# Kernel tuning notes

Measured on AMD Instinct MI355X. Metric: run time of the kernel, lower is better.

## Reference

```python
import jax, jax.numpy as jnp
import numpy as np

EPS = 1e-5  # torch LayerNorm default


def _ln(x, g, b):
    m = jnp.mean(x, axis=-1, keepdims=True)
    v = jnp.var(x, axis=-1, keepdims=True)
    return (x - m) * jax.lax.rsqrt(v + EPS) * g + b


def _attn(x, ctx, wq, wk, wv, wo, bo, num_heads):
    # weights stored [in, out]; equivalent to torch Linear (y = x @ W^T + b)
    B, T, _ = x.shape
    S = ctx.shape[1]
    E = wq.shape[1]
    hd = E // num_heads
    q = (x @ wq).reshape(B, T, num_heads, hd)
    k = (ctx @ wk).reshape(B, S, num_heads, hd)
    v = (ctx @ wv).reshape(B, S, num_heads, hd)
    scores = jnp.einsum('bthd,bshd->bhts', q, k) / np.sqrt(hd).astype(x.dtype)
    p = jax.nn.softmax(scores, axis=-1)
    o = jnp.einsum('bhts,bshd->bthd', p, v).reshape(B, T, E)
    return o @ wo + bo


def _ffn(x, w1, b1, w2, b2):
    h = jax.nn.gelu(x @ w1 + b1, approximate=False)  # torch nn.GELU default is exact
    return h @ w2 + b2  # Dropout(0.1) is identity in eval mode


def setup_inputs() -> dict:
    key = jax.random.key(0)
    H, CD, FF = 1024, 768, 4096
    ks = jax.random.split(key, 20)
    s = 0.02
    inp = {
        'x': jax.random.normal(ks[0], (4, 1024, H), jnp.float32),
        'context': jax.random.normal(ks[1], (4, 77, CD), jnp.float32),
        # self-attention params
        'sq_w': jax.random.normal(ks[2], (H, H), jnp.float32) * s,
        'sk_w': jax.random.normal(ks[3], (H, H), jnp.float32) * s,
        'sv_w': jax.random.normal(ks[4], (H, H), jnp.float32) * s,
        'so_w': jax.random.normal(ks[5], (H, H), jnp.float32) * s,
        'so_b': jnp.zeros((H,), jnp.float32),
        # cross-attention params
        'cq_w': jax.random.normal(ks[6], (H, H), jnp.float32) * s,
        'ck_w': jax.random.normal(ks[7], (CD, H), jnp.float32) * s,
        'cv_w': jax.random.normal(ks[8], (CD, H), jnp.float32) * s,
        'co_w': jax.random.normal(ks[9], (H, H), jnp.float32) * s,
        'co_b': jnp.zeros((H,), jnp.float32),
        # layer norms 1-4
        'n1_g': jnp.ones((H,), jnp.float32), 'n1_b': jnp.zeros((H,), jnp.float32),
        'n2_g': jnp.ones((H,), jnp.float32), 'n2_b': jnp.zeros((H,), jnp.float32),
        'n3_g': jnp.ones((H,), jnp.float32), 'n3_b': jnp.zeros((H,), jnp.float32),
        'n4_g': jnp.ones((H,), jnp.float32), 'n4_b': jnp.zeros((H,), jnp.float32),
        # FFNs
        'f1_w1': jax.random.normal(ks[10], (H, FF), jnp.float32) * s,
        'f1_b1': jnp.zeros((FF,), jnp.float32),
        'f1_w2': jax.random.normal(ks[11], (FF, H), jnp.float32) * s,
        'f1_b2': jnp.zeros((H,), jnp.float32),
        'f2_w1': jax.random.normal(ks[12], (H, FF), jnp.float32) * s,
        'f2_b1': jnp.zeros((FF,), jnp.float32),
        'f2_w2': jax.random.normal(ks[13], (FF, H), jnp.float32) * s,
        'f2_b2': jnp.zeros((H,), jnp.float32),
    }
    return inp


def reference(x, context,
              sq_w, sk_w, sv_w, so_w, so_b,
              cq_w, ck_w, cv_w, co_w, co_b,
              n1_g, n1_b, n2_g, n2_b, n3_g, n3_b, n4_g, n4_b,
              f1_w1, f1_b1, f1_w2, f1_b2,
              f2_w1, f2_b1, f2_w2, f2_b2):
    NUM_HEADS = 16
    # self-attention branch
    x = _attn(_ln(x, n1_g, n1_b), _ln(x, n1_g, n1_b), sq_w, sk_w, sv_w, so_w, so_b, NUM_HEADS) + x
    x = _ffn(_ln(x, n2_g, n2_b), f1_w1, f1_b1, f1_w2, f1_b2) + x
    # cross-attention branch
    x = _attn(_ln(x, n3_g, n3_b), context, cq_w, ck_w, cv_w, co_w, co_b, NUM_HEADS) + x
    x = _ffn(_ln(x, n4_g, n4_b), f2_w1, f2_b1, f2_w2, f2_b2) + x
    return x
```

## Files before the change

kernel.cpp:

```cpp
#include <hip/hip_runtime.h>
#include <cstdint>
#include <cstddef>

typedef unsigned short u16;
typedef __attribute__((ext_vector_type(8))) short short8;
typedef __attribute__((ext_vector_type(4))) float floatx4;

typedef const __attribute__((address_space(1))) void g_void;
typedef __attribute__((address_space(3))) void l_void;

__device__ __forceinline__ float b2f(u16 u) {
    union { unsigned int i; float f; } v; v.i = ((unsigned int)u) << 16; return v.f;
}
__device__ __forceinline__ u16 f2b(float f) {
    union { float f; unsigned int i; } v; v.f = f;
    unsigned int x = v.i;
    return (u16)((x + 0x7fffu + ((x >> 16) & 1u)) >> 16);
}
__device__ __forceinline__ float gelu_exact(float x) {
    return 0.5f * x * (1.0f + erff(x * 0.70710678118654752440f));
}

__global__ void sniff_kernel(const u16* __restrict__ x, int* __restrict__ flag) {
    int lane = threadIdx.x;
    int sane = 0;
    for (int i = lane * 2; i < 4096; i += 128) {
        int e = (x[i] >> 7) & 0xff;
        if (e >= 100 && e <= 140) sane++;
    }
#pragma unroll
    for (int off = 32; off; off >>= 1) sane += __shfl_xor(sane, off, 64);
    if (lane == 0) *flag = (sane * 2 >= 2048) ? 0 : 1;
}

__global__ __launch_bounds__(256) void cvt_bf_kernel(const void* __restrict__ in,
                                                     u16* __restrict__ out, int n4,
                                                     const int* __restrict__ flag) {
    int i = blockIdx.x * 256 + threadIdx.x;
    if (i >= n4) return;
    bool isf = (*flag != 0);
    uint2 pk;
    if (isf) {
        float4 v = ((const float4*)in)[i];
        pk.x = (unsigned)f2b(v.x) | ((unsigned)f2b(v.y) << 16);
        pk.y = (unsigned)f2b(v.z) | ((unsigned)f2b(v.w) << 16);
    } else {
        pk = ((const uint2*)in)[i];
    }
    ((uint2*)out)[i] = pk;
}

struct TEnt { const void* src; u16* dst; int R, C, tiles_x, tiles; };
struct TPack { TEnt e[12]; };

__global__ __launch_bounds__(256) void transpose_batch_kernel(TPack p, const int* __restrict__ flag) {
    TEnt e = p.e[blockIdx.y];
    if ((int)blockIdx.x >= e.tiles) return;
    __shared__ u16 t[32][33];
    bool isf = (*flag != 0);
    int tx = threadIdx.x, ty = threadIdx.y;
    int c0 = (blockIdx.x % e.tiles_x) * 32;
    int r0 = (blockIdx.x / e.tiles_x) * 32;
#pragma unroll
    for (int i = 0; i < 4; i++) {
        size_t idx = (size_t)(r0 + ty + i * 8) * e.C + c0 + tx;
        t[ty + i * 8][tx] = isf ? f2b(((const float*)e.src)[idx]) : ((const u16*)e.src)[idx];
    }
    __syncthreads();
#pragma unroll
    for (int i = 0; i < 4; i++)
        e.dst[(size_t)(c0 + ty + i * 8) * e.R + r0 + tx] = t[tx][ty + i * 8];
}

__global__ __launch_bounds__(256) void ln_kernel(const void* __restrict__ x,
                                                 float* __restrict__ xout,
                                                 const void* __restrict__ g,
                                                 const void* __restrict__ bb,
                                                 u16* __restrict__ out,
                                                 const int* __restrict__ flag,
                                                 int raw) {
    const int row = blockIdx.x;
    const int tid = threadIdx.x;
    const int lane = tid & 63, wave = tid >> 6;
    bool isf = (*flag != 0);
    size_t base = (size_t)row * 1024 + tid * 4;
    float4 xv;
    if (raw && !isf) {
        uint2 w = ((const uint2*)x)[base >> 2];
        xv.x = b2f((u16)(w.x & 0xffff)); xv.y = b2f((u16)(w.x >> 16));
        xv.z = b2f((u16)(w.y & 0xffff)); xv.w = b2f((u16)(w.y >> 16));
    } else {
        xv = ((const float4*)x)[base >> 2];
    }
    if (raw) ((float4*)xout)[base >> 2] = xv;
    float s  = xv.x + xv.y + xv.z + xv.w;
    float s2 = xv.x * xv.x + xv.y * xv.y + xv.z * xv.z + xv.w * xv.w;
#pragma unroll
    for (int off = 32; off; off >>= 1) {
        s  += __shfl_xor(s, off, 64);
        s2 += __shfl_xor(s2, off, 64);
    }
    __shared__ float red[8];
    if (lane == 0) { red[wave] = s; red[4 + wave] = s2; }
    __syncthreads();
    s  = red[0] + red[1] + red[2] + red[3];
    s2 = red[4] + red[5] + red[6] + red[7];
    const float inv_n = 1.0f / 1024.0f;
    float mean = s * inv_n;
    float var  = s2 * inv_n - mean * mean;
    float rstd = rsqrtf(var + 1e-5f);
    float gv[4], bv[4];
    if (isf) {
        float4 gg = *(const float4*)((const float*)g + tid * 4);
        float4 bo = *(const float4*)((const float*)bb + tid * 4);
        gv[0] = gg.x; gv[1] = gg.y; gv[2] = gg.z; gv[3] = gg.w;
        bv[0] = bo.x; bv[1] = bo.y; bv[2] = bo.z; bv[3] = bo.w;
    } else {
        uint2 go = *(const uint2*)((const u16*)g + tid * 4);
        uint2 bo = *(const uint2*)((const u16*)bb + tid * 4);
        gv[0] = b2f((u16)(go.x & 0xffff)); gv[1] = b2f((u16)(go.x >> 16));
        gv[2] = b2f((u16)(go.y & 0xffff)); gv[3] = b2f((u16)(go.y >> 16));
        bv[0] = b2f((u16)(bo.x & 0xffff)); bv[1] = b2f((u16)(bo.x >> 16));
        bv[2] = b2f((u16)(bo.y & 0xffff)); bv[3] = b2f((u16)(bo.y >> 16));
    }
    float xa[4] = { xv.x, xv.y, xv.z, xv.w };
    u16 o[4];
#pragma unroll
    for (int j = 0; j < 4; j++)
        o[j] = f2b((xa[j] - mean) * rstd * gv[j] + bv[j]);
    uint2 pk;
    pk.x = (unsigned)o[0] | ((unsigned)o[1] << 16);
    pk.y = (unsigned)o[2] | ((unsigned)o[3] << 16);
    *(uint2*)(out + base) = pk;
}

template <int MODE, int MT, int NT, int BK, int MINW>
__global__ __launch_bounds__(256, MINW) void gemm_kernel(const u16* __restrict__ A,
                                                         const u16* __restrict__ BT,
                                                         const void* __restrict__ bias,
                                                         const float* __restrict__ res,
                                                         void* __restrict__ Cout,
                                                         int M, int N, int K,
                                                         const int* __restrict__ flag) {
    constexpr int CB  = BK / 8;
    constexpr int CBM = CB - 1;
    constexpr int RPC = 256 / CB;
    constexpr int CPG = 32 / RPC;
    __shared__ __align__(16) u16 lsA[MT * 32 * BK];
    __shared__ __align__(16) u16 lsB[NT * 32 * BK];
    const int tid = threadIdx.x;
    const int lane = tid & 63;
    const int wave = tid >> 6;
    const int wm = (wave >> 1) * (MT * 16);
    const int wn = (wave & 1) * (NT * 16);
    const int bm = blockIdx.y * (MT * 32);
    const int bn = blockIdx.x * (NT * 32);
    const int l16 = lane & 15;
    const int lq = lane >> 4;
    const bool isf = (*flag != 0);

    floatx4 acc[MT][NT] = {};

    const int r_in = tid / CB;
    const int cb_log = ((tid & CBM) - r_in) & CBM;
    const int gcol = cb_log * 8;

    const u16* gA[MT * CPG];
#pragma unroll
    for (int j = 0; j < MT; j++)
#pragma unroll
        for (int c = 0; c < CPG; c++) {
            int rr = bm + j * 32 + c * RPC + r_in; if (rr >= M) rr = M - 1;
            gA[j * CPG + c] = A + (size_t)rr * K + gcol;
        }
    const u16* gB[NT * CPG];
#pragma unroll
    for (int j = 0; j < NT; j++)
#pragma unroll
        for (int c = 0; c < CPG; c++) {
            int rr = bn + j * 32 + c * RPC + r_in; if (rr >= N) rr = N - 1;
            gB[j * CPG + c] = BT + (size_t)rr * K + gcol;
        }

    for (int k0 = 0; k0 < K; k0 += BK) {
#pragma unroll
        for (int j = 0; j < MT; j++)
#pragma unroll
            for (int c = 0; c < CPG; c++)
                __builtin_amdgcn_global_load_lds((g_void*)(gA[j * CPG + c] + k0),
                                                 (l_void*)(lsA + (j * 32 + c * RPC) * BK + tid * 8), 16, 0, 0);
#pragma unroll
        for (int j = 0; j < NT; j++)
#pragma unroll
            for (int c = 0; c < CPG; c++)
                __builtin_amdgcn_global_load_lds((g_void*)(gB[j * CPG + c] + k0),
                                                 (l_void*)(lsB + (j * 32 + c * RPC) * BK + tid * 8), 16, 0, 0);
        __syncthreads();

#pragma unroll
        for (int ki = 0; ki < BK / 32; ki++) {
            short8 af[MT], bf[NT];
#pragma unroll
            for (int mi = 0; mi < MT; mi++) {
                int ra = wm + mi * 16 + l16;
                af[mi] = *(const short8*)&lsA[ra * BK + ((ki * 4 + lq + ra) & CBM) * 8];
            }
#pragma unroll
            for (int ni = 0; ni < NT; ni++) {
                int rb = wn + ni * 16 + l16;
                bf[ni] = *(const short8*)&lsB[rb * BK + ((ki * 4 + lq + rb) & CBM) * 8];
            }
#pragma unroll
            for (int mi = 0; mi < MT; mi++)
#pragma unroll
                for (int ni = 0; ni < NT; ni++)
                    acc[mi][ni] = __builtin_amdgcn_mfma_f32_16x16x32_bf16(af[mi], bf[ni], acc[mi][ni], 0, 0, 0);
        }
        __syncthreads();
    }

#pragma unroll
    for (int mi = 0; mi < MT; mi++) {
#pragma unroll
        for (int ni = 0; ni < NT; ni++) {
            int col = bn + wn + ni * 16 + l16;
            float bv = 0.0f;
            if (bias) bv = isf ? ((const float*)bias)[col] : b2f(((const u16*)bias)[col]);
#pragma unroll
            for (int r = 0; r < 4; r++) {
                int row = bm + wm + mi * 16 + lq * 4 + r;
                if (row < M) {
                    float v = acc[mi][ni][r] + bv;
                    size_t idx = (size_t)row * N + col;
                    if (MODE == 1) v = gelu_exact(v);
                    if (MODE == 2 || MODE == 3) v += res[idx];
                    if (MODE == 2)       ((float*)Cout)[idx] = v;
                    else if (MODE == 3) { if (isf) ((float*)Cout)[idx] = v; else ((u16*)Cout)[idx] = f2b(v); }
                    else                 ((u16*)Cout)[idx] = f2b(v);
                }
            }
        }
    }
}

__global__ __launch_bounds__(256, 2) void attn_mfma_kernel(const u16* __restrict__ q,
                                                           const u16* __restrict__ k,
                                                           const u16* __restrict__ v,
                                                           u16* __restrict__ o,
                                                           int T, int S, int ldq, int ldkv,
                                                           float cexp) {
    const int E = 1024;
    const int b = blockIdx.y >> 4, h = blockIdx.y & 15;
    const int tid = threadIdx.x, wave = tid >> 6, lane = tid & 63;
    const int l16 = lane & 15, lq = lane >> 4;

    __shared__ __align__(16) u16 Qs[128 * 64];
    __shared__ __align__(16) u16 Ks[64 * 64];
    __shared__ __align__(16) u16 Vt[64 * 72];
    __shared__ __align__(16) u16 Ps[4][16 * 72];

    const int q0 = blockIdx.x * 128;
    const int r8 = tid >> 3;
    const int cb_log = ((tid & 7) - r8) & 7;
    const int rv = tid >> 2, cv = (tid & 3) * 16;
    const int cbv = ((rv >> 3) ^ (tid & 3)) & 7;

#pragma unroll
    for (int j = 0; j < 4; j++) {
        int row = q0 + j * 32 + r8;
        __builtin_amdgcn_global_load_lds((g_void*)(q + (size_t)(b * T + row) * ldq + h * 64 + cb_log * 8),
                                         (l_void*)(Qs + j * 2048 + tid * 8), 16, 0, 0);
    }
    __syncthreads();

    short8 af[2][2];
#pragma unroll
    for (int j = 0; j < 2; j++) {
        int qr = j * 64 + wave * 16 + l16;
        af[j][0] = *(const short8*)&Qs[qr * 64 + ((lq + qr) & 7) * 8];
        af[j][1] = *(const short8*)&Qs[qr * 64 + ((lq + 4 + qr) & 7) * 8];
    }

    float lsum[2][4] = {};
    floatx4 oacc[2][4] = {};

    const int ntiles = (S + 63) >> 6;
    for (int t = 0; t < ntiles; t++) {
        const int s0 = t * 64;
        __syncthreads();
#pragma unroll
        for (int j = 0; j < 2; j++) {
            int srow = s0 + j * 32 + r8; if (srow >= S) srow = S - 1;
            __builtin_amdgcn_global_load_lds((g_void*)(k + (size_t)(b * S + srow) * ldkv + h * 64 + cb_log * 8),
                                             (l_void*)(Ks + j * 2048 + tid * 8), 16, 0, 0);
        }
        {
            int sr = s0 + rv; if (sr >= S) sr = S - 1;
            const u16* vsrc = v + (size_t)(b * S + sr) * ldkv + h * 64 + cv;
            uint4 v0 = *(const uint4*)vsrc;
            uint4 v1 = *(const uint4*)(vsrc + 8);
            const u16* vp = (const u16*)&v0;
#pragma unroll
            for (int j = 0; j < 8; j++)
                Vt[(cv + j) * 72 + cbv * 8 + (rv & 7)] = vp[j];
            vp = (const u16*)&v1;
#pragma unroll
            for (int j = 0; j < 8; j++)
                Vt[(cv + 8 + j) * 72 + cbv * 8 + (rv & 7)] = vp[j];
        }
        __syncthreads();

        const bool tail = (s0 + 64 > S);
#pragma unroll
        for (int j = 0; j < 2; j++) {
            floatx4 sc[4];
#pragma unroll
            for (int nt = 0; nt < 4; nt++) {
                int krow = nt * 16 + l16;
                short8 bf0 = *(const short8*)&Ks[krow * 64 + ((lq + krow) & 7) * 8];
                short8 bf1 = *(const short8*)&Ks[krow * 64 + ((lq + 4 + krow) & 7) * 8];
                floatx4 z = {};
                z = __builtin_amdgcn_mfma_f32_16x16x32_bf16(af[j][0], bf0, z, 0, 0, 0);
                z = __builtin_amdgcn_mfma_f32_16x16x32_bf16(af[j][1], bf1, z, 0, 0, 0);
                sc[nt] = z;
            }
#pragma unroll
            for (int nt = 0; nt < 4; nt++) {
                bool colv = !tail || (s0 + nt * 16 + l16 < S);
#pragma unroll
                for (int r = 0; r < 4; r++) {
                    float p = exp2f(sc[nt][r] * cexp);
                    p = colv ? p : 0.0f;
                    lsum[j][r] += p;
                    Ps[wave][(lq * 4 + r) * 72 + nt * 16 + l16] = f2b(p);
                }
            }
            short8 av0 = *(const short8*)&Ps[wave][l16 * 72 + lq * 8];
            short8 av1 = *(const short8*)&Ps[wave][l16 * 72 + 32 + lq * 8];
#pragma unroll
            for (int dt = 0; dt < 4; dt++) {
                int d = dt * 16 + l16;
                short8 bv0 = *(const short8*)&Vt[d * 72 + ((lq ^ dt) & 7) * 8];
                short8 bv1 = *(const short8*)&Vt[d * 72 + (((4 + lq) ^ dt) & 7) * 8];
                oacc[j][dt] = __builtin_amdgcn_mfma_f32_16x16x32_bf16(av0, bv0, oacc[j][dt], 0, 0, 0);
                oacc[j][dt] = __builtin_amdgcn_mfma_f32_16x16x32_bf16(av1, bv1, oacc[j][dt], 0, 0, 0);
            }
        }
    }

#pragma unroll
    for (int j = 0; j < 2; j++)
#pragma unroll
        for (int r = 0; r < 4; r++) {
#pragma unroll
            for (int off = 1; off < 16; off <<= 1)
                lsum[j][r] += __shfl_xor(lsum[j][r], off, 64);
        }

#pragma unroll
    for (int j = 0; j < 2; j++)
#pragma unroll
        for (int r = 0; r < 4; r++) {
            float inv = 1.0f / lsum[j][r];
            int row = q0 + j * 64 + wave * 16 + lq * 4 + r;
            u16* dst = o + (size_t)(b * T + row) * E + h * 64 + l16;
#pragma unroll
            for (int dt = 0; dt < 4; dt++)
                dst[dt * 16] = f2b(oacc[j][dt][r] * inv);
        }
}

extern "C" void kernel_launch(void* const* d_in, const int* in_sizes, int n_in,
                              void* d_out, int out_size, void* d_ws, size_t ws_size,
                              hipStream_t stream) {
    const void* x_in = d_in[0];
    const void* ctx  = d_in[1];
    const void* sq_w = d_in[2];
    const void* sk_w = d_in[3];
    const void* sv_w = d_in[4];
    const void* so_w = d_in[5];
    const void* so_b = d_in[6];
    const void* cq_w = d_in[7];
    const void* ck_w = d_in[8];
    const void* cv_w = d_in[9];
    const void* co_w = d_in[10];
    const void* co_b = d_in[11];
    const void* n1_g = d_in[12];
    const void* n1_b = d_in[13];
    const void* n2_g = d_in[14];
    const void* n2_b = d_in[15];
    const void* n3_g = d_in[16];
    const void* n3_b = d_in[17];
    const void* n4_g = d_in[18];
    const void* n4_b = d_in[19];
    const void* f1_w1 = d_in[20];
    const void* f1_b1 = d_in[21];
    const void* f1_w2 = d_in[22];
    const void* f1_b2 = d_in[23];
    const void* f2_w1 = d_in[24];
    const void* f2_b1 = d_in[25];
    const void* f2_w2 = d_in[26];
    const void* f2_b2 = d_in[27];

    const int B = 4, T = 1024, H = 1024, FF = 4096, CD = 768, S = 77;
    const int BT_ = B * T;
    const int BS_ = B * S;

    char* ws = (char*)d_ws;
    size_t off = 0;
    auto alloc = [&](size_t bytes) { char* p = ws + off; off += (bytes + 255) & ~(size_t)255; return p; };
    int*   flag = (int*)alloc(256);
    u16*   ctxb = (u16*)alloc((size_t)BS_ * CD * 2);
    float* xcur = (float*)alloc((size_t)BT_ * H * 4);
    const size_t MEL = 1024 * 1024;
    u16* wqkv = (u16*)alloc(3 * MEL * 2);
    u16* wso  = (u16*)alloc(MEL * 2);
    u16* wcq  = (u16*)alloc(MEL * 2);
    u16* wckv = (u16*)alloc((size_t)2 * H * CD * 2);
    u16* wco  = (u16*)alloc(MEL * 2);
    u16* wf1a = (u16*)alloc((size_t)H * FF * 2);
    u16* wf1b = (u16*)alloc((size_t)H * FF * 2);
    u16* wf2a = (u16*)alloc((size_t)H * FF * 2);
    u16* wf2b = (u16*)alloc((size_t)H * FF * 2);
    u16* U    = (u16*)alloc((size_t)40 * 1024 * 1024);
    (void)ws_size; (void)n_in; (void)in_sizes; (void)out_size;

    const size_t AEL = (size_t)BT_ * H;
    u16* lnb  = U;
    u16* qkvb = U + AEL;
    u16* ob   = U + 4 * AEL;
    u16* hb   = U + AEL;
    u16* qb   = U + AEL;
    u16* kvb  = U + 2 * AEL;

    TPack tp;
    auto ent = [&](int i, const void* src, u16* dst, int R, int C) {
        tp.e[i] = TEnt{ src, dst, R, C, C / 32, (C / 32) * (R / 32) };
    };
    ent(0,  sq_w, wqkv,           H,  H);
    ent(1,  sk_w, wqkv + MEL,     H,  H);
    ent(2,  sv_w, wqkv + 2 * MEL, H,  H);
    ent(3,  so_w, wso,            H,  H);
    ent(4,  cq_w, wcq,            H,  H);
    ent(5,  ck_w, wckv,           CD, H);
    ent(6,  cv_w, wckv + (size_t)H * CD, CD, H);
    ent(7,  co_w, wco,            H,  H);
    ent(8,  f1_w1, wf1a,          H,  FF);
    ent(9,  f1_w2, wf1b,          FF, H);
    ent(10, f2_w1, wf2a,          H,  FF);
    ent(11, f2_w2, wf2b,          FF, H);

    const dim3 g_qkv(3072 / 128, BT_ / 128);
    const dim3 g_ff(FF / 128, BT_ / 128);
    const dim3 g_n1024(H / 64, BT_ / 64);
    const dim3 g_ckv(2048 / 64, (BS_ + 63) / 64);
    const dim3 attn_grid(T / 128, B * 16);
    const float cexp = 0.125f * 1.4426950408889634f;

    sniff_kernel<<<1, 64, 0, stream>>>((const u16*)x_in, flag);
    cvt_bf_kernel<<<(BS_ * CD / 4 + 255) / 256, 256, 0, stream>>>(ctx, ctxb, BS_ * CD / 4, flag);
    transpose_batch_kernel<<<dim3(4096, 12), dim3(32, 8), 0, stream>>>(tp, flag);

    ln_kernel<<<BT_, 256, 0, stream>>>(x_in, xcur, n1_g, n1_b, lnb, flag, 1);
    gemm_kernel<0, 4, 4, 64, 3><<<g_qkv, 256, 0, stream>>>(lnb, wqkv, nullptr, nullptr, qkvb, BT_, 3072, H, flag);
    attn_mfma_kernel<<<attn_grid, 256, 0, stream>>>(qkvb, qkvb + 1024, qkvb + 2048, ob, T, T, 3072, 3072, cexp);
    gemm_kernel<2, 2, 2, 128, 4><<<g_n1024, 256, 0, stream>>>(ob, wso, so_b, xcur, xcur, BT_, H, H, flag);

    ln_kernel<<<BT_, 256, 0, stream>>>(xcur, nullptr, n2_g, n2_b, lnb, flag, 0);
    gemm_kernel<1, 4, 4, 64, 3><<<g_ff, 256, 0, stream>>>(lnb, wf1a, f1_b1, nullptr, hb, BT_, FF, H, flag);
    gemm_kernel<2, 2, 2, 128, 4><<<g_n1024, 256, 0, stream>>>(hb, wf1b, f1_b2, xcur, xcur, BT_, H, FF, flag);

    ln_kernel<<<BT_, 256, 0, stream>>>(xcur, nullptr, n3_g, n3_b, lnb, flag, 0);
    gemm_kernel<0, 2, 2, 128, 4><<<g_n1024, 256, 0, stream>>>(lnb, wcq, nullptr, nullptr, qb, BT_, H, H, flag);
    gemm_kernel<0, 2, 2, 128, 4><<<g_ckv, 256, 0, stream>>>(ctxb, wckv, nullptr, nullptr, kvb, BS_, 2048, CD, flag);
    attn_mfma_kernel<<<attn_grid, 256, 0, stream>>>(qb, kvb, kvb + 1024, ob, T, S, 1024, 2048, cexp);
    gemm_kernel<2, 2, 2, 128, 4><<<g_n1024, 256, 0, stream>>>(ob, wco, co_b, xcur, xcur, BT_, H, H, flag);

    ln_kernel<<<BT_, 256, 0, stream>>>(xcur, nullptr, n4_g, n4_b, lnb, flag, 0);
    gemm_kernel<1, 4, 4, 64, 3><<<g_ff, 256, 0, stream>>>(lnb, wf2a, f2_b1, nullptr, hb, BT_, FF, H, flag);
    gemm_kernel<3, 2, 2, 128, 4><<<g_n1024, 256, 0, stream>>>(hb, wf2b, f2_b2, xcur, d_out, BT_, H, FF, flag);
}
```

Measured before the change: 645.4 us.

## Double-buffer LDS in N=1024 GEMMs and switch them to 128x128 tiles

Adds a DEPTH template parameter. At depth 2 the GEMM keeps two LDS buffers and issues the global-to-LDS loads for the next K tile before computing the current one, with one barrier per iteration instead of two. The N=1024 GEMMs (out-projections, FFN down-projections, cross Q) move from 64x64 tiles with BK=128 to 128x128 tiles with BK=64 and this pipelined path. Larger tiles give more reuse, but the grid drops to 256 blocks, and the doubled LDS may limit occupancy.

```diff
diff --git a/kernel.cpp b/kernel.cpp
--- a/kernel.cpp
+++ b/kernel.cpp
@@ -134,7 +134,7 @@
     *(uint2*)(out + base) = pk;
 }
 
-template <int MODE, int MT, int NT, int BK, int MINW>
+template <int MODE, int MT, int NT, int BK, int MINW, int DEPTH>
 __global__ __launch_bounds__(256, MINW) void gemm_kernel(const u16* __restrict__ A,
                                                          const u16* __restrict__ BT,
                                                          const void* __restrict__ bias,
@@ -146,8 +146,9 @@
     constexpr int CBM = CB - 1;
     constexpr int RPC = 256 / CB;
     constexpr int CPG = 32 / RPC;
-    __shared__ __align__(16) u16 lsA[MT * 32 * BK];
-    __shared__ __align__(16) u16 lsB[NT * 32 * BK];
+    constexpr int NB  = (DEPTH > 1) ? 2 : 1;
+    __shared__ __align__(16) u16 lsA[NB][MT * 32 * BK];
+    __shared__ __align__(16) u16 lsB[NB][NT * 32 * BK];
     const int tid = threadIdx.x;
     const int lane = tid & 63;
     const int wave = tid >> 6;
@@ -182,41 +183,62 @@
             gB[j * CPG + c] = BT + (size_t)rr * K + gcol;
         }
 
-    for (int k0 = 0; k0 < K; k0 += BK) {
+    auto stage = [&](int bf, int k0) {
 #pragma unroll
         for (int j = 0; j < MT; j++)
 #pragma unroll
             for (int c = 0; c < CPG; c++)
                 __builtin_amdgcn_global_load_lds((g_void*)(gA[j * CPG + c] + k0),
-                                                 (l_void*)(lsA + (j * 32 + c * RPC) * BK + tid * 8), 16, 0, 0);
+                                                 (l_void*)(&lsA[bf][(j * 32 + c * RPC) * BK + tid * 8]), 16, 0, 0);
 #pragma unroll
         for (int j = 0; j < NT; j++)
 #pragma unroll
             for (int c = 0; c < CPG; c++)
                 __builtin_amdgcn_global_load_lds((g_void*)(gB[j * CPG + c] + k0),
-                                                 (l_void*)(lsB + (j * 32 + c * RPC) * BK + tid * 8), 16, 0, 0);
-        __syncthreads();
-
+                                                 (l_void*)(&lsB[bf][(j * 32 + c * RPC) * BK + tid * 8]), 16, 0, 0);
+    };
+
+    auto compute = [&](int bf) {
 #pragma unroll
         for (int ki = 0; ki < BK / 32; ki++) {
-            short8 af[MT], bf[NT];
+            short8 af[MT], bfr[NT];
 #pragma unroll
             for (int mi = 0; mi < MT; mi++) {
                 int ra = wm + mi * 16 + l16;
-                af[mi] = *(const short8*)&lsA[ra * BK + ((ki * 4 + lq + ra) & CBM) * 8];
+                af[mi] = *(const short8*)&lsA[bf][ra * BK + ((ki * 4 + lq + ra) & CBM) * 8];
             }
 #pragma unroll
             for (int ni = 0; ni < NT; ni++) {
                 int rb = wn + ni * 16 + l16;
-                bf[ni] = *(const short8*)&lsB[rb * BK + ((ki * 4 + lq + rb) & CBM) * 8];
+                bfr[ni] = *(const short8*)&lsB[bf][rb * BK + ((ki * 4 + lq + rb) & CBM) * 8];
             }
 #pragma unroll
             for (int mi = 0; mi < MT; mi++)
 #pragma unroll
                 for (int ni = 0; ni < NT; ni++)
-                    acc[mi][ni] = __builtin_amdgcn_mfma_f32_16x16x32_bf16(af[mi], bf[ni], acc[mi][ni], 0, 0, 0);
-        }
-        __syncthreads();
+                    acc[mi][ni] = __builtin_amdgcn_mfma_f32_16x16x32_bf16(af[mi], bfr[ni], acc[mi][ni], 0, 0, 0);
+        }
+    };
+
+    if constexpr (DEPTH > 1) {
+        stage(0, 0);
+        asm volatile("s_waitcnt vmcnt(0)" ::: "memory");
+        __builtin_amdgcn_s_barrier();
+        const int nk = K / BK;
+        for (int t = 0; t < nk; t++) {
+            const int cur = t & 1;
+            if (t + 1 < nk) stage(cur ^ 1, (t + 1) * BK);
+            compute(cur);
+            asm volatile("s_waitcnt vmcnt(0)" ::: "memory");
+            __builtin_amdgcn_s_barrier();
+        }
+    } else {
+        for (int k0 = 0; k0 < K; k0 += BK) {
+            stage(0, k0);
+            __syncthreads();
+            compute(0);
+            __syncthreads();
+        }
     }
 
 #pragma unroll
@@ -452,7 +474,7 @@
 
     const dim3 g_qkv(3072 / 128, BT_ / 128);
     const dim3 g_ff(FF / 128, BT_ / 128);
-    const dim3 g_n1024(H / 64, BT_ / 64);
+    const dim3 g_h128(H / 128, BT_ / 128);
     const dim3 g_ckv(2048 / 64, (BS_ + 63) / 64);
     const dim3 attn_grid(T / 128, B * 16);
     const float cexp = 0.125f * 1.4426950408889634f;
@@ -462,21 +484,21 @@
     transpose_batch_kernel<<<dim3(4096, 12), dim3(32, 8), 0, stream>>>(tp, flag);
 
     ln_kernel<<<BT_, 256, 0, stream>>>(x_in, xcur, n1_g, n1_b, lnb, flag, 1);
-    gemm_kernel<0, 4, 4, 64, 3><<<g_qkv, 256, 0, stream>>>(lnb, wqkv, nullptr, nullptr, qkvb, BT_, 3072, H, flag);
+    gemm_kernel<0, 4, 4, 64, 3, 1><<<g_qkv, 256, 0, stream>>>(lnb, wqkv, nullptr, nullptr, qkvb, BT_, 3072, H, flag);
     attn_mfma_kernel<<<attn_grid, 256, 0, stream>>>(qkvb, qkvb + 1024, qkvb + 2048, ob, T, T, 3072, 3072, cexp);
-    gemm_kernel<2, 2, 2, 128, 4><<<g_n1024, 256, 0, stream>>>(ob, wso, so_b, xcur, xcur, BT_, H, H, flag);
+    gemm_kernel<2, 4, 4, 64, 2, 2><<<g_h128, 256, 0, stream>>>(ob, wso, so_b, xcur, xcur, BT_, H, H, flag);
 
     ln_kernel<<<BT_, 256, 0, stream>>>(xcur, nullptr, n2_g, n2_b, lnb, flag, 0);
-    gemm_kernel<1, 4, 4, 64, 3><<<g_ff, 256, 0, stream>>>(lnb, wf1a, f1_b1, nullptr, hb, BT_, FF, H, flag);
-    gemm_kernel<2, 2, 2, 128, 4><<<g_n1024, 256, 0, stream>>>(hb, wf1b, f1_b2, xcur, xcur, BT_, H, FF, flag);
+    gemm_kernel<1, 4, 4, 64, 3, 1><<<g_ff, 256, 0, stream>>>(lnb, wf1a, f1_b1, nullptr, hb, BT_, FF, H, flag);
+    gemm_kernel<2, 4, 4, 64, 2, 2><<<g_h128, 256, 0, stream>>>(hb, wf1b, f1_b2, xcur, xcur, BT_, H, FF, flag);
 
     ln_kernel<<<BT_, 256, 0, stream>>>(xcur, nullptr, n3_g, n3_b, lnb, flag, 0);
-    gemm_kernel<0, 2, 2, 128, 4><<<g_n1024, 256, 0, stream>>>(lnb, wcq, nullptr, nullptr, qb, BT_, H, H, flag);
-    gemm_kernel<0, 2, 2, 128, 4><<<g_ckv, 256, 0, stream>>>(ctxb, wckv, nullptr, nullptr, kvb, BS_, 2048, CD, flag);
+    gemm_kernel<0, 4, 4, 64, 2, 2><<<g_h128, 256, 0, stream>>>(lnb, wcq, nullptr, nullptr, qb, BT_, H, H, flag);
+    gemm_kernel<0, 2, 2, 128, 4, 1><<<g_ckv, 256, 0, stream>>>(ctxb, wckv, nullptr, nullptr, kvb, BS_, 2048, CD, flag);
     attn_mfma_kernel<<<attn_grid, 256, 0, stream>>>(qb, kvb, kvb + 1024, ob, T, S, 1024, 2048, cexp);
-    gemm_kernel<2, 2, 2, 128, 4><<<g_n1024, 256, 0, stream>>>(ob, wco, co_b, xcur, xcur, BT_, H, H, flag);
+    gemm_kernel<2, 4, 4, 64, 2, 2><<<g_h128, 256, 0, stream>>>(ob, wco, co_b, xcur, xcur, BT_, H, H, flag);
 
     ln_kernel<<<BT_, 256, 0, stream>>>(xcur, nullptr, n4_g, n4_b, lnb, flag, 0);
-    gemm_kernel<1, 4, 4, 64, 3><<<g_ff, 256, 0, stream>>>(lnb, wf2a, f2_b1, nullptr, hb, BT_, FF, H, flag);
-    gemm_kernel<3, 2, 2, 128, 4><<<g_n1024, 256, 0, stream>>>(hb, wf2b, f2_b2, xcur, d_out, BT_, H, FF, flag);
-}
+    gemm_kernel<1, 4, 4, 64, 3, 1><<<g_ff, 256, 0, stream>>>(lnb, wf2a, f2_b1, nullptr, hb, BT_, FF, H, flag);
+    gemm_kernel<3, 4, 4, 64, 2, 2><<<g_h128, 256, 0, stream>>>(hb, wf2b, f2_b2, xcur, d_out, BT_, H, FF, flag);
+}
```

Result: slower. 741.1 us (+14.8%).
